# Kernel optimization log

Hardware: AMD Instinct MI355X
Metric: run time of the kernel (lower is better)

The kernel has to match this reference:

```python
import jax, jax.numpy as jnp
import numpy as np

BS, V, J = 256, 10475, 55
NSHAPE, NEXP = 300, 50

# SMPLX kinematic tree (fixed model constant)
PARENTS = np.array([
    -1, 0, 0, 0, 1, 2, 3, 4, 5, 6, 7, 8, 9, 9, 9, 12, 13, 14, 16, 17, 18, 19,
    15, 15, 15,
    20, 25, 26, 20, 28, 29, 20, 31, 32, 20, 34, 35, 20, 37, 38,
    21, 40, 41, 21, 43, 44, 21, 46, 47, 21, 49, 50, 21, 52, 53], dtype=np.int64)


def batch_rodrigues(rvec):
    # rvec: [N,3] axis-angle -> [N,3,3] rotation matrices
    angle = jnp.linalg.norm(rvec + 1e-8, axis=-1, keepdims=True)  # [N,1]
    axis = rvec / angle
    x, y, z = axis[..., 0], axis[..., 1], axis[..., 2]
    zr = jnp.zeros_like(x)
    K = jnp.stack([zr, -z, y, z, zr, -x, -y, x, zr], axis=-1).reshape(-1, 3, 3)
    s = jnp.sin(angle)[..., None]
    c = jnp.cos(angle)[..., None]
    I = jnp.eye(3, dtype=rvec.dtype)
    return I + s * K + (1.0 - c) * (K @ K)


def setup_inputs():
    key = jax.random.key(0)
    ks = jax.random.split(key, 9)
    pose = 0.2 * jax.random.normal(ks[0], (BS, 53, 3), jnp.float32)
    shape = jax.random.normal(ks[1], (BS, 10), jnp.float32)
    expression = jax.random.normal(ks[2], (BS, NEXP), jnp.float32)
    global_orient = 0.2 * jax.random.normal(ks[3], (1, 3), jnp.float32)
    v_template = jax.random.normal(ks[4], (V, 3), jnp.float32)
    shapedirs = 0.01 * jax.random.normal(ks[5], (V, 3, NSHAPE + NEXP), jnp.float32)
    posedirs = 0.01 * jax.random.normal(ks[6], (486, V * 3), jnp.float32)
    J_regressor = jax.random.uniform(ks[7], (J, V), jnp.float32)
    J_regressor = J_regressor / jnp.sum(J_regressor, axis=1, keepdims=True)
    lbs_weights = jax.random.uniform(ks[8], (V, J), jnp.float32)
    lbs_weights = lbs_weights / jnp.sum(lbs_weights, axis=1, keepdims=True)
    return {"pose": pose, "shape": shape, "expression": expression,
            "global_orient": global_orient, "v_template": v_template,
            "shapedirs": shapedirs, "posedirs": posedirs,
            "J_regressor": J_regressor, "lbs_weights": lbs_weights}


def lbs(betas, rot_mats, v_template, shapedirs, posedirs, J_regressor, lbs_weights):
    bs = betas.shape[0]
    dt = betas.dtype
    # shape blendshapes
    v_shaped = v_template[None] + jnp.einsum('bl,vcl->bvc', betas, shapedirs)
    # rest-pose joints
    joints = jnp.einsum('jv,bvc->bjc', J_regressor, v_shaped)  # [b,J,3]
    # pose blendshapes
    I3 = jnp.eye(3, dtype=dt)
    pose_feature = (rot_mats[:, 1:] - I3).reshape(bs, -1)  # [b,(J-1)*9]
    v_posed = v_shaped + jnp.einsum('bp,pn->bn', pose_feature, posedirs).reshape(bs, V, 3)
    # forward kinematics along the tree
    rel_joints = jnp.concatenate(
        [joints[:, :1], joints[:, 1:] - joints[:, PARENTS[1:]]], axis=1)
    top = jnp.concatenate([rot_mats, rel_joints[..., None]], axis=-1)  # [b,J,3,4]
    bot = jnp.broadcast_to(jnp.array([0, 0, 0, 1], dtype=dt), (bs, J, 1, 4))
    T_local = jnp.concatenate([top, bot], axis=-2)  # [b,J,4,4]
    A_list = [T_local[:, 0]]
    for j in range(1, J):  # fixed 55-joint chain
        A_list.append(A_list[int(PARENTS[j])] @ T_local[:, j])
    A = jnp.stack(A_list, axis=1)  # [b,J,4,4]
    posed_joints = A[..., :3, 3]
    # subtract rest-pose contribution
    corr = jnp.einsum('bjmn,bjn->bjm', A[..., :3, :3], joints)
    A_rel = A.at[..., :3, 3].add(-corr)
    # vertex skinning
    T = jnp.einsum('vj,bjmn->bvmn', lbs_weights, A_rel)  # [b,V,4,4]
    verts = jnp.einsum('bvmn,bvn->bvm', T[..., :3, :3], v_posed) + T[..., :3, 3]
    return verts, posed_joints


def reference(pose, shape, expression, global_orient, v_template, shapedirs,
              posedirs, J_regressor, lbs_weights):
    bs = pose.shape[0]
    dt = pose.dtype
    go = jnp.broadcast_to(global_orient[:, None, :], (bs, 1, 3))
    eyes = jnp.zeros((bs, 2, 3), dtype=dt)  # leye/reye fixed at zero
    # order: global, body(21), jaw, leye, reye, lhand(15), rhand(15) -> 55
    full_pose = jnp.concatenate(
        [go, pose[:, 1:22], pose[:, 52:53], eyes, pose[:, 22:37], pose[:, 37:52]],
        axis=1)
    betas = jnp.concatenate(
        [shape, jnp.zeros((bs, NSHAPE - shape.shape[1]), dtype=dt), expression],
        axis=1)  # [b,350]
    rot_mats = batch_rodrigues(full_pose.reshape(-1, 3)).reshape(bs, J, 3, 3)
    verts, joints = lbs(betas, rot_mats, v_template, shapedirs, posedirs,
                        J_regressor, lbs_weights)
    return verts, joints
```

## Files before the change

### kernel.cpp

```cpp
#include <hip/hip_runtime.h>
#include <math.h>

#define BS 256
#define V 10475
#define NJ 55
#define R3 31425
#define NP 486
#define LB 60
#define KP 576
#define VK 10496
#define JOFF 8044800

typedef __attribute__((ext_vector_type(8))) short short8;
typedef __attribute__((ext_vector_type(4))) float float4_;

__device__ const int PARENTS_d[NJ] = {
  -1, 0, 0, 0, 1, 2, 3, 4, 5, 6, 7, 8, 9, 9, 9, 12, 13, 14, 16, 17, 18, 19,
  15, 15, 15, 20, 25, 26, 20, 28, 29, 20, 31, 32, 20, 34, 35, 20, 37, 38,
  21, 40, 41, 21, 43, 44, 21, 46, 47, 21, 49, 50, 21, 52, 53
};

__device__ __forceinline__ unsigned short f2b(float f) {
  unsigned int u = __float_as_uint(f);
  unsigned int r = (u + 0x7FFFu + ((u >> 16) & 1u)) >> 16;
  return (unsigned short)r;
}

__global__ __launch_bounds__(256) void k_pose(
    const float* __restrict__ pose, const float* __restrict__ shp,
    const float* __restrict__ expr, const float* __restrict__ go,
    float* __restrict__ rot_ws, unsigned short* __restrict__ Ftr,
    float* __restrict__ betas_T) {
  int b = threadIdx.x;
  int j = blockIdx.x;
  if (j == NJ) {
    #pragma unroll
    for (int l = 0; l < 10; ++l) {
      float v = shp[b * 10 + l];
      betas_T[l * BS + b] = v;
      Ftr[(size_t)b * KP + NP + l] = f2b(v);
    }
    #pragma unroll
    for (int l = 0; l < 50; ++l) {
      float v = expr[b * 50 + l];
      betas_T[(10 + l) * BS + b] = v;
      Ftr[(size_t)b * KP + NP + 10 + l] = f2b(v);
    }
    #pragma unroll
    for (int l = NP + LB; l < KP; ++l) Ftr[(size_t)b * KP + l] = 0;
    return;
  }
  float rx, ry, rz;
  if (j == 0) { rx = go[0]; ry = go[1]; rz = go[2]; }
  else if (j == 23 || j == 24) { rx = 0.f; ry = 0.f; rz = 0.f; }
  else {
    int src = (j <= 21) ? j : (j == 22 ? 52 : j - 3);
    const float* p = pose + ((size_t)b * 53 + src) * 3;
    rx = p[0]; ry = p[1]; rz = p[2];
  }
  float sx = rx + 1e-8f, sy = ry + 1e-8f, sz = rz + 1e-8f;
  float ang = sqrtf(sx * sx + sy * sy + sz * sz);
  float inv = 1.f / ang;
  float x = rx * inv, y = ry * inv, z = rz * inv;
  float s = sinf(ang), c = cosf(ang), C = 1.f - c;
  float R[9];
  R[0] = 1.f - C * (y * y + z * z);
  R[1] = -s * z + C * x * y;
  R[2] =  s * y + C * x * z;
  R[3] =  s * z + C * x * y;
  R[4] = 1.f - C * (x * x + z * z);
  R[5] = -s * x + C * y * z;
  R[6] = -s * y + C * x * z;
  R[7] =  s * x + C * y * z;
  R[8] = 1.f - C * (x * x + y * y);
  float* rw = rot_ws + ((size_t)b * NJ + j) * 9;
  #pragma unroll
  for (int e = 0; e < 9; ++e) rw[e] = R[e];
  if (j >= 1) {
    int pb = (j - 1) * 9;
    #pragma unroll
    for (int e = 0; e < 9; ++e)
      Ftr[(size_t)b * KP + pb + e] =
          f2b(R[e] - ((e == 0 || e == 4 || e == 8) ? 1.f : 0.f));
  }
}

__global__ __launch_bounds__(256) void k_jregb(
    const float* __restrict__ Jreg, unsigned short* __restrict__ Jregb) {
  size_t idx = (size_t)blockIdx.x * 256 + threadIdx.x;
  int j = (int)(idx / VK);
  int v = (int)(idx - (size_t)j * VK);
  float val = (j < NJ && v < V) ? Jreg[(size_t)j * V + v] : 0.f;
  Jregb[idx] = f2b(val);
}

__global__ __launch_bounds__(256) void k_trX(
    const float* __restrict__ sd, const float* __restrict__ vt,
    unsigned short* __restrict__ XbT) {
  __shared__ float tile[192][65];
  int t = threadIdx.x;
  int v0 = blockIdx.x * 64;
  #pragma unroll 1
  for (int c = 0; c < 3; ++c) {
    for (int idx = t; idx < 3840; idx += 256) {
      int v_l = idx / 60, col = idx - v_l * 60;
      int v = v0 + v_l;
      int cidx = (col < 10) ? col : 290 + col;
      float val = (v < V) ? sd[((size_t)v * 3 + c) * 350 + cidx] : 0.f;
      tile[c * 64 + col][v_l] = val;
    }
  }
  for (int idx = t; idx < 768; idx += 256) {
    int v_l = idx & 63, rr = idx >> 6;
    int c = rr >> 2, l = 60 + (rr & 3);
    int v = v0 + v_l;
    float val = (l == 60 && v < V) ? vt[(size_t)v * 3 + c] : 0.f;
    tile[c * 64 + l][v_l] = val;
  }
  __syncthreads();
  for (int idx = t; idx < 192 * 64; idx += 256) {
    int cl = idx >> 6, v_l = idx & 63;
    XbT[(size_t)cl * VK + v0 + v_l] = f2b(tile[cl][v_l]);
  }
}

__global__ __launch_bounds__(256) void k_jsm(
    const unsigned short* __restrict__ Jregb,
    const unsigned short* __restrict__ XbT, float* __restrict__ JS) {
  int lane = threadIdx.x & 63;
  int wv = threadIdx.x >> 6;
  int l15 = lane & 15, q = lane >> 4;
  int k0 = blockIdx.x * 128;
  const unsigned short* ap = Jregb + (size_t)(wv * 16 + l15) * VK + k0 + q * 8;
  float4_ acc[12];
  #pragma unroll
  for (int nt = 0; nt < 12; ++nt) acc[nt] = (float4_)0.f;
  #pragma unroll
  for (int ks = 0; ks < 4; ++ks) {
    short8 a = *(const short8*)(ap + ks * 32);
    #pragma unroll
    for (int nt = 0; nt < 12; ++nt) {
      const unsigned short* bp =
          XbT + (size_t)(nt * 16 + l15) * VK + k0 + ks * 32 + q * 8;
      short8 b = *(const short8*)bp;
      acc[nt] = __builtin_amdgcn_mfma_f32_16x16x32_bf16(a, b, acc[nt], 0, 0, 0);
    }
  }
  #pragma unroll
  for (int nt = 0; nt < 12; ++nt) {
    int cl = nt * 16 + l15;
    int c = cl >> 6, l = cl & 63;
    if (l < 61) {
      #pragma unroll
      for (int reg = 0; reg < 4; ++reg) {
        int jj = wv * 16 + q * 4 + reg;
        if (jj < NJ)
          atomicAdd(&JS[((size_t)jj * 3 + c) * 61 + l], acc[nt][reg]);
      }
    }
  }
}

__global__ __launch_bounds__(256) void k_trD(
    const float* __restrict__ pd, const float* __restrict__ sd,
    unsigned short* __restrict__ Dtr) {
  __shared__ float tile[64 * 68];
  int t = threadIdx.x;
  int rt = blockIdx.x, kt = blockIdx.y;
  int r0 = rt * 64;
  int c = (t & 15) * 4;
  #pragma unroll
  for (int s = 0; s < 4; ++s) {
    int k_l = (t >> 4) + 16 * s;
    int kg = kt * 64 + k_l;
    float v0 = 0.f, v1 = 0.f, v2 = 0.f, v3 = 0.f;
    int r = r0 + c;
    if (kg < NP) {
      if (r + 3 < R3) {
        const float* p = pd + (size_t)kg * R3 + r;
        v0 = p[0]; v1 = p[1]; v2 = p[2]; v3 = p[3];
      } else {
        const float* p = pd + (size_t)kg * R3;
        if (r < R3)     v0 = p[r];
        if (r + 1 < R3) v1 = p[r + 1];
        if (r + 2 < R3) v2 = p[r + 2];
        if (r + 3 < R3) v3 = p[r + 3];
      }
    } else if (kg < NP + LB) {
      int ll = kg - NP;
      int cidx = (ll < 10) ? ll : (290 + ll);
      if (r < R3)     v0 = sd[(size_t)(r) * 350 + cidx];
      if (r + 1 < R3) v1 = sd[(size_t)(r + 1) * 350 + cidx];
      if (r + 2 < R3) v2 = sd[(size_t)(r + 2) * 350 + cidx];
      if (r + 3 < R3) v3 = sd[(size_t)(r + 3) * 350 + cidx];
    }
    float* tp = tile + k_l * 68 + c;
    tp[0] = v0; tp[1] = v1; tp[2] = v2; tp[3] = v3;
  }
  __syncthreads();
  int r_l = t >> 2, a = t & 3;
  unsigned short h[16];
  #pragma unroll
  for (int i = 0; i < 16; ++i) h[i] = f2b(tile[(a * 16 + i) * 68 + r_l]);
  unsigned short* dp = Dtr + (size_t)(r0 + r_l) * KP + kt * 64 + a * 16;
  #pragma unroll
  for (int i = 0; i < 16; ++i) dp[i] = h[i];
}

__global__ __launch_bounds__(256) void k_wb(
    const float* __restrict__ lbs, unsigned short* __restrict__ Wb) {
  int v0 = blockIdx.x * 16;
  for (int idx = threadIdx.x; idx < 1024; idx += 256) {
    int v_l = idx >> 6, k = idx & 63;
    int v = v0 + v_l;
    float val = (k < NJ && v < V) ? lbs[(size_t)v * NJ + k] : 0.f;
    Wb[(size_t)v * 64 + k] = f2b(val);
  }
}

__global__ __launch_bounds__(64) void k_chain(
    const float* __restrict__ JS, const float* __restrict__ betas_T,
    const float* __restrict__ rot_ws, unsigned short* __restrict__ arelb,
    float* __restrict__ out) {
  int b = blockIdx.x;
  int lane = threadIdx.x;
  __shared__ float joints_l[165];
  __shared__ float Tl[880];
  __shared__ float A[880];
  for (int idx = lane; idx < 165; idx += 64) {
    float sacc = JS[idx * 61 + 60];
    #pragma unroll
    for (int l = 0; l < LB; ++l) sacc += JS[idx * 61 + l] * betas_T[l * BS + b];
    joints_l[idx] = sacc;
  }
  __syncthreads();
  for (int idx = lane; idx < 880; idx += 64) {
    int j = idx >> 4, e = idx & 15, r = e >> 2, cc = e & 3;
    float val;
    if (r < 3) {
      if (cc < 3) val = rot_ws[((size_t)b * NJ + j) * 9 + r * 3 + cc];
      else {
        int par = PARENTS_d[j];
        val = joints_l[j * 3 + r] - (par >= 0 ? joints_l[par * 3 + r] : 0.f);
      }
    } else val = (cc == 3) ? 1.f : 0.f;
    Tl[idx] = val;
  }
  __syncthreads();
  if (lane < 16) A[lane] = Tl[lane];
  __syncthreads();
  for (int j = 1; j < NJ; ++j) {
    int par = PARENTS_d[j];
    if (lane < 16) {
      int r = lane >> 2, cc = lane & 3;
      float sacc = 0.f;
      #pragma unroll
      for (int k = 0; k < 4; ++k)
        sacc += A[par * 16 + r * 4 + k] * Tl[j * 16 + k * 4 + cc];
      A[j * 16 + lane] = sacc;
    }
    __syncthreads();
  }
  for (int idx = lane; idx < 165; idx += 64) {
    int j = idx / 3, r = idx % 3;
    out[JOFF + (size_t)b * 165 + idx] = A[j * 16 + r * 4 + 3];
  }
  for (int idx = lane; idx < 1024; idx += 64) {
    int n = idx >> 6, k = idx & 63;
    float val = 0.f;
    if (n < 12 && k < NJ) {
      int m = n >> 2, cc = n & 3;
      if (cc < 3) val = A[k * 16 + m * 4 + cc];
      else {
        val = A[k * 16 + m * 4 + 3]
            - (A[k * 16 + m * 4 + 0] * joints_l[k * 3 + 0] +
               A[k * 16 + m * 4 + 1] * joints_l[k * 3 + 1] +
               A[k * 16 + m * 4 + 2] * joints_l[k * 3 + 2]);
      }
    }
    arelb[(size_t)b * 1024 + idx] = f2b(val);
  }
}

__global__ __launch_bounds__(256) void k_gemm(
    const float* __restrict__ vt, const unsigned short* __restrict__ Ftr,
    const unsigned short* __restrict__ Dtr, float* __restrict__ out) {
  int lane = threadIdx.x & 63;
  int wv = threadIdx.x >> 6;
  int l15 = lane & 15, q = lane >> 4;
  int r0 = blockIdx.x * 64;
  int m0 = wv * 64;
  float4_ acc[4][4];
  #pragma unroll
  for (int mt = 0; mt < 4; ++mt)
    #pragma unroll
    for (int nt = 0; nt < 4; ++nt) acc[mt][nt] = (float4_)0.f;

  const unsigned short* aBase[4];
  const unsigned short* bBase[4];
  #pragma unroll
  for (int mt = 0; mt < 4; ++mt)
    aBase[mt] = Ftr + (size_t)(m0 + mt * 16 + l15) * KP + q * 8;
  #pragma unroll
  for (int nt = 0; nt < 4; ++nt)
    bBase[nt] = Dtr + (size_t)(r0 + nt * 16 + l15) * KP + q * 8;

  short8 af[4], bf[4], an[4], bn[4];
  #pragma unroll
  for (int mt = 0; mt < 4; ++mt) af[mt] = *(const short8*)(aBase[mt]);
  #pragma unroll
  for (int nt = 0; nt < 4; ++nt) bf[nt] = *(const short8*)(bBase[nt]);

  #pragma unroll 1
  for (int kk = 0; kk < 18; ++kk) {
    if (kk < 17) {
      int off = (kk + 1) * 32;
      #pragma unroll
      for (int mt = 0; mt < 4; ++mt) an[mt] = *(const short8*)(aBase[mt] + off);
      #pragma unroll
      for (int nt = 0; nt < 4; ++nt) bn[nt] = *(const short8*)(bBase[nt] + off);
    }
    #pragma unroll
    for (int mt = 0; mt < 4; ++mt)
      #pragma unroll
      for (int nt = 0; nt < 4; ++nt)
        acc[mt][nt] = __builtin_amdgcn_mfma_f32_16x16x32_bf16(
            af[mt], bf[nt], acc[mt][nt], 0, 0, 0);
    #pragma unroll
    for (int mt = 0; mt < 4; ++mt) af[mt] = an[mt];
    #pragma unroll
    for (int nt = 0; nt < 4; ++nt) bf[nt] = bn[nt];
  }

  #pragma unroll
  for (int nt = 0; nt < 4; ++nt) {
    int r = r0 + nt * 16 + l15;
    if (r < R3) {
      float vtv = vt[r];
      #pragma unroll
      for (int mt = 0; mt < 4; ++mt) {
        int bb = m0 + mt * 16 + q * 4;
        #pragma unroll
        for (int reg = 0; reg < 4; ++reg)
          out[(size_t)(bb + reg) * R3 + r] = acc[mt][nt][reg] + vtv;
      }
    }
  }
}

__global__ __launch_bounds__(256) void k_skin(
    const unsigned short* __restrict__ Wb, const unsigned short* __restrict__ arelb,
    float* __restrict__ out) {
  __shared__ float Tls[4 * 320];
  int lane = threadIdx.x & 63;
  int wv = threadIdx.x >> 6;
  int l15 = lane & 15, q = lane >> 4;
  int v0 = blockIdx.x * 16;
  int bbase = blockIdx.y * 64 + wv * 16;
  float* tb = Tls + wv * 320;

  const unsigned short* wp = Wb + (size_t)(v0 + l15) * 64 + q * 8;
  short8 a0 = *(const short8*)(wp);
  short8 a1 = *(const short8*)(wp + 32);

  int v = v0 + l15;
  int m = q;
  #pragma unroll 1
  for (int bi = 0; bi < 16; ++bi) {
    int b = bbase + bi;
    const unsigned short* bp = arelb + (size_t)b * 1024 + l15 * 64 + q * 8;
    short8 b0 = *(const short8*)(bp);
    short8 b1 = *(const short8*)(bp + 32);
    float4_ acc = (float4_)0.f;
    acc = __builtin_amdgcn_mfma_f32_16x16x32_bf16(a0, b0, acc, 0, 0, 0);
    acc = __builtin_amdgcn_mfma_f32_16x16x32_bf16(a1, b1, acc, 0, 0, 0);
    #pragma unroll
    for (int reg = 0; reg < 4; ++reg) tb[(q * 4 + reg) * 20 + l15] = acc[reg];
    __builtin_amdgcn_s_waitcnt(0);
    float4_ T4 = *(float4_*)(&tb[l15 * 20 + m * 4]);
    if (m < 3 && v < V) {
      float* vp = out + (size_t)b * R3 + v * 3;
      float x = vp[0], y = vp[1], z = vp[2];
      float val = T4[0] * x + T4[1] * y + T4[2] * z + T4[3];
      vp[m] = val;
    }
  }
}

extern "C" void kernel_launch(void* const* d_in, const int* in_sizes, int n_in,
                              void* d_out, int out_size, void* d_ws, size_t ws_size,
                              hipStream_t stream) {
  const float* pose = (const float*)d_in[0];
  const float* shp  = (const float*)d_in[1];
  const float* expr = (const float*)d_in[2];
  const float* go   = (const float*)d_in[3];
  const float* vt   = (const float*)d_in[4];
  const float* sd   = (const float*)d_in[5];
  const float* pd   = (const float*)d_in[6];
  const float* jr   = (const float*)d_in[7];
  const float* lbs  = (const float*)d_in[8];
  float* out = (float*)d_out;
  float* ws  = (float*)d_ws;

  float* betas_T        = ws;
  float* rot_ws         = ws + 15360;
  float* JS             = ws + 142080;
  unsigned short* Ftr   = (unsigned short*)(ws + 152160);
  unsigned short* arelb = (unsigned short*)(ws + 225888);
  unsigned short* Wb    = (unsigned short*)(ws + 356960);
  unsigned short* Jregb = (unsigned short*)(ws + 692320);
  unsigned short* XbT   = (unsigned short*)(ws + 1028192);
  unsigned short* Dtr   = (unsigned short*)(ws + 2035808);

  hipMemsetAsync(JS, 0, 10080 * sizeof(float), stream);
  k_pose<<<NJ + 1, 256, 0, stream>>>(pose, shp, expr, go, rot_ws, Ftr, betas_T);
  k_jregb<<<(64 * VK) / 256, 256, 0, stream>>>(jr, Jregb);
  k_trX<<<VK / 64, 256, 0, stream>>>(sd, vt, XbT);
  k_jsm<<<VK / 128, 256, 0, stream>>>(Jregb, XbT, JS);
  k_trD<<<dim3(492, 9), 256, 0, stream>>>(pd, sd, Dtr);
  k_wb<<<655, 256, 0, stream>>>(lbs, Wb);
  k_chain<<<BS, 64, 0, stream>>>(JS, betas_T, rot_ws, arelb, out);
  k_gemm<<<492, 256, 0, stream>>>(vt, Ftr, Dtr, out);
  k_skin<<<dim3(655, 4), 256, 0, stream>>>(Wb, arelb, out);
}
```

Baseline: 337.6 us.

## Fuse posedirs transpose into GEMM via LDS double-buffer and restructure skinning

Drops the separate k_trD kernel that wrote a bf16 transposed copy of posedirs and shapedirs. The GEMM now streams fp32 posedirs/shapedirs tiles straight into double-buffered shared memory and converts them to bf16 as it builds the MFMA operands, which removes one full write and re-read of the intermediate. The skinning kernel is also reorganised: four waves cover different vertices, the next bone-transform fragment is prefetched, and the MFMA result is used directly instead of going through shared memory. The cost is a __syncthreads per K chunk and strided uncoalesced shapedirs reads inside the GEMM, and k_wb is enlarged so Wb covers padded vertices.

```diff
diff --git a/kernel.cpp b/kernel.cpp
--- a/kernel.cpp
+++ b/kernel.cpp
@@ -10,6 +10,7 @@
 #define KP 576
 #define VK 10496
 #define JOFF 8044800
+#define DSP 66
 
 typedef __attribute__((ext_vector_type(8))) short short8;
 typedef __attribute__((ext_vector_type(4))) float float4_;
@@ -161,52 +162,6 @@
   }
 }
 
-__global__ __launch_bounds__(256) void k_trD(
-    const float* __restrict__ pd, const float* __restrict__ sd,
-    unsigned short* __restrict__ Dtr) {
-  __shared__ float tile[64 * 68];
-  int t = threadIdx.x;
-  int rt = blockIdx.x, kt = blockIdx.y;
-  int r0 = rt * 64;
-  int c = (t & 15) * 4;
-  #pragma unroll
-  for (int s = 0; s < 4; ++s) {
-    int k_l = (t >> 4) + 16 * s;
-    int kg = kt * 64 + k_l;
-    float v0 = 0.f, v1 = 0.f, v2 = 0.f, v3 = 0.f;
-    int r = r0 + c;
-    if (kg < NP) {
-      if (r + 3 < R3) {
-        const float* p = pd + (size_t)kg * R3 + r;
-        v0 = p[0]; v1 = p[1]; v2 = p[2]; v3 = p[3];
-      } else {
-        const float* p = pd + (size_t)kg * R3;
-        if (r < R3)     v0 = p[r];
-        if (r + 1 < R3) v1 = p[r + 1];
-        if (r + 2 < R3) v2 = p[r + 2];
-        if (r + 3 < R3) v3 = p[r + 3];
-      }
-    } else if (kg < NP + LB) {
-      int ll = kg - NP;
-      int cidx = (ll < 10) ? ll : (290 + ll);
-      if (r < R3)     v0 = sd[(size_t)(r) * 350 + cidx];
-      if (r + 1 < R3) v1 = sd[(size_t)(r + 1) * 350 + cidx];
-      if (r + 2 < R3) v2 = sd[(size_t)(r + 2) * 350 + cidx];
-      if (r + 3 < R3) v3 = sd[(size_t)(r + 3) * 350 + cidx];
-    }
-    float* tp = tile + k_l * 68 + c;
-    tp[0] = v0; tp[1] = v1; tp[2] = v2; tp[3] = v3;
-  }
-  __syncthreads();
-  int r_l = t >> 2, a = t & 3;
-  unsigned short h[16];
-  #pragma unroll
-  for (int i = 0; i < 16; ++i) h[i] = f2b(tile[(a * 16 + i) * 68 + r_l]);
-  unsigned short* dp = Dtr + (size_t)(r0 + r_l) * KP + kt * 64 + a * 16;
-  #pragma unroll
-  for (int i = 0; i < 16; ++i) dp[i] = h[i];
-}
-
 __global__ __launch_bounds__(256) void k_wb(
     const float* __restrict__ lbs, unsigned short* __restrict__ Wb) {
   int v0 = blockIdx.x * 16;
@@ -214,7 +169,7 @@
     int v_l = idx >> 6, k = idx & 63;
     int v = v0 + v_l;
     float val = (k < NJ && v < V) ? lbs[(size_t)v * NJ + k] : 0.f;
-    Wb[(size_t)v * 64 + k] = f2b(val);
+    if (v < VK) Wb[(size_t)v * 64 + k] = f2b(val);
   }
 }
 
@@ -283,13 +238,19 @@
 }
 
 __global__ __launch_bounds__(256) void k_gemm(
-    const float* __restrict__ vt, const unsigned short* __restrict__ Ftr,
-    const unsigned short* __restrict__ Dtr, float* __restrict__ out) {
-  int lane = threadIdx.x & 63;
-  int wv = threadIdx.x >> 6;
+    const float* __restrict__ vt, const float* __restrict__ sd,
+    const float* __restrict__ pd, const unsigned short* __restrict__ Ftr,
+    float* __restrict__ out) {
+  __shared__ float dsb[2][32 * DSP];
+  int t = threadIdx.x;
+  int lane = t & 63, wv = t >> 6;
   int l15 = lane & 15, q = lane >> 4;
   int r0 = blockIdx.x * 64;
   int m0 = wv * 64;
+  int k_l = t >> 3;
+  int c8 = (t & 7) * 8;
+  bool full = (r0 + 64 <= R3);
+
   float4_ acc[4][4];
   #pragma unroll
   for (int mt = 0; mt < 4; ++mt)
@@ -297,39 +258,86 @@
     for (int nt = 0; nt < 4; ++nt) acc[mt][nt] = (float4_)0.f;
 
   const unsigned short* aBase[4];
-  const unsigned short* bBase[4];
   #pragma unroll
   for (int mt = 0; mt < 4; ++mt)
     aBase[mt] = Ftr + (size_t)(m0 + mt * 16 + l15) * KP + q * 8;
-  #pragma unroll
-  for (int nt = 0; nt < 4; ++nt)
-    bBase[nt] = Dtr + (size_t)(r0 + nt * 16 + l15) * KP + q * 8;
-
-  short8 af[4], bf[4], an[4], bn[4];
-  #pragma unroll
-  for (int mt = 0; mt < 4; ++mt) af[mt] = *(const short8*)(aBase[mt]);
-  #pragma unroll
-  for (int nt = 0; nt < 4; ++nt) bf[nt] = *(const short8*)(bBase[nt]);
+
+  {
+    int kg = k_l;
+    float* dp = &dsb[0][k_l * DSP + c8];
+    if (full) {
+      const float* p = pd + (size_t)kg * R3 + r0 + c8;
+      #pragma unroll
+      for (int i = 0; i < 8; ++i) dp[i] = p[i];
+    } else {
+      #pragma unroll
+      for (int i = 0; i < 8; ++i) {
+        int r = r0 + c8 + i;
+        dp[i] = (r < R3) ? pd[(size_t)kg * R3 + r] : 0.f;
+      }
+    }
+  }
+  __syncthreads();
 
   #pragma unroll 1
-  for (int kk = 0; kk < 18; ++kk) {
-    if (kk < 17) {
-      int off = (kk + 1) * 32;
-      #pragma unroll
-      for (int mt = 0; mt < 4; ++mt) an[mt] = *(const short8*)(aBase[mt] + off);
-      #pragma unroll
-      for (int nt = 0; nt < 4; ++nt) bn[nt] = *(const short8*)(bBase[nt] + off);
-    }
+  for (int c = 0; c < 18; ++c) {
+    int cur = c & 1;
+    float sv[8];
+    if (c < 17) {
+      int kg = (c + 1) * 32 + k_l;
+      if (kg < NP) {
+        if (full) {
+          const float* p = pd + (size_t)kg * R3 + r0 + c8;
+          #pragma unroll
+          for (int i = 0; i < 8; ++i) sv[i] = p[i];
+        } else {
+          #pragma unroll
+          for (int i = 0; i < 8; ++i) {
+            int r = r0 + c8 + i;
+            sv[i] = (r < R3) ? pd[(size_t)kg * R3 + r] : 0.f;
+          }
+        }
+      } else if (kg < NP + LB) {
+        int ll = kg - NP;
+        int cidx = (ll < 10) ? ll : (290 + ll);
+        #pragma unroll
+        for (int i = 0; i < 8; ++i) {
+          int r = r0 + c8 + i;
+          sv[i] = (r < R3) ? sd[(size_t)r * 350 + cidx] : 0.f;
+        }
+      } else {
+        #pragma unroll
+        for (int i = 0; i < 8; ++i) sv[i] = 0.f;
+      }
+    }
+    short8 bf[4];
+    #pragma unroll
+    for (int nt = 0; nt < 4; ++nt) {
+      unsigned short h[8];
+      #pragma unroll
+      for (int i = 0; i < 8; ++i)
+        h[i] = f2b(dsb[cur][(q * 8 + i) * DSP + nt * 16 + l15]);
+      short8 v;
+      #pragma unroll
+      for (int i = 0; i < 8; ++i) v[i] = (short)h[i];
+      bf[nt] = v;
+    }
+    short8 af[4];
+    #pragma unroll
+    for (int mt = 0; mt < 4; ++mt)
+      af[mt] = *(const short8*)(aBase[mt] + c * 32);
     #pragma unroll
     for (int mt = 0; mt < 4; ++mt)
       #pragma unroll
       for (int nt = 0; nt < 4; ++nt)
         acc[mt][nt] = __builtin_amdgcn_mfma_f32_16x16x32_bf16(
             af[mt], bf[nt], acc[mt][nt], 0, 0, 0);
-    #pragma unroll
-    for (int mt = 0; mt < 4; ++mt) af[mt] = an[mt];
-    #pragma unroll
-    for (int nt = 0; nt < 4; ++nt) bf[nt] = bn[nt];
+    if (c < 17) {
+      float* dp = &dsb[cur ^ 1][k_l * DSP + c8];
+      #pragma unroll
+      for (int i = 0; i < 8; ++i) dp[i] = sv[i];
+    }
+    __syncthreads();
   }
 
   #pragma unroll
@@ -351,39 +359,39 @@
 __global__ __launch_bounds__(256) void k_skin(
     const unsigned short* __restrict__ Wb, const unsigned short* __restrict__ arelb,
     float* __restrict__ out) {
-  __shared__ float Tls[4 * 320];
   int lane = threadIdx.x & 63;
   int wv = threadIdx.x >> 6;
   int l15 = lane & 15, q = lane >> 4;
-  int v0 = blockIdx.x * 16;
-  int bbase = blockIdx.y * 64 + wv * 16;
-  float* tb = Tls + wv * 320;
-
-  const unsigned short* wp = Wb + (size_t)(v0 + l15) * 64 + q * 8;
-  short8 a0 = *(const short8*)(wp);
-  short8 a1 = *(const short8*)(wp + 32);
-
-  int v = v0 + l15;
-  int m = q;
+  int v = blockIdx.x * 64 + wv * 16 + l15;
+  bool vok = (v < V);
+  int b0 = blockIdx.y * 16;
+
+  const unsigned short* wp = Wb + (size_t)v * 64 + q * 8;
+  short8 w0 = *(const short8*)(wp);
+  short8 w1 = *(const short8*)(wp + 32);
+
+  const unsigned short* ap = arelb + (size_t)b0 * 1024 + l15 * 64 + q * 8;
+  short8 a0 = *(const short8*)ap;
+  short8 a1 = *(const short8*)(ap + 32);
+
   #pragma unroll 1
   for (int bi = 0; bi < 16; ++bi) {
-    int b = bbase + bi;
-    const unsigned short* bp = arelb + (size_t)b * 1024 + l15 * 64 + q * 8;
-    short8 b0 = *(const short8*)(bp);
-    short8 b1 = *(const short8*)(bp + 32);
+    int b = b0 + bi;
+    float* vp = out + (size_t)b * R3 + v * 3;
+    float x = 0.f, y = 0.f, z = 0.f;
+    if (vok && q < 3) { x = vp[0]; y = vp[1]; z = vp[2]; }
+    short8 na0 = a0, na1 = a1;
+    if (bi < 15) {
+      const unsigned short* np = arelb + (size_t)(b + 1) * 1024 + l15 * 64 + q * 8;
+      na0 = *(const short8*)np;
+      na1 = *(const short8*)(np + 32);
+    }
     float4_ acc = (float4_)0.f;
-    acc = __builtin_amdgcn_mfma_f32_16x16x32_bf16(a0, b0, acc, 0, 0, 0);
-    acc = __builtin_amdgcn_mfma_f32_16x16x32_bf16(a1, b1, acc, 0, 0, 0);
-    #pragma unroll
-    for (int reg = 0; reg < 4; ++reg) tb[(q * 4 + reg) * 20 + l15] = acc[reg];
-    __builtin_amdgcn_s_waitcnt(0);
-    float4_ T4 = *(float4_*)(&tb[l15 * 20 + m * 4]);
-    if (m < 3 && v < V) {
-      float* vp = out + (size_t)b * R3 + v * 3;
-      float x = vp[0], y = vp[1], z = vp[2];
-      float val = T4[0] * x + T4[1] * y + T4[2] * z + T4[3];
-      vp[m] = val;
-    }
+    acc = __builtin_amdgcn_mfma_f32_16x16x32_bf16(a0, w0, acc, 0, 0, 0);
+    acc = __builtin_amdgcn_mfma_f32_16x16x32_bf16(a1, w1, acc, 0, 0, 0);
+    if (vok && q < 3)
+      vp[q] = acc[0] * x + acc[1] * y + acc[2] * z + acc[3];
+    a0 = na0; a1 = na1;
   }
 }
 
@@ -408,18 +416,16 @@
   unsigned short* Ftr   = (unsigned short*)(ws + 152160);
   unsigned short* arelb = (unsigned short*)(ws + 225888);
   unsigned short* Wb    = (unsigned short*)(ws + 356960);
-  unsigned short* Jregb = (unsigned short*)(ws + 692320);
-  unsigned short* XbT   = (unsigned short*)(ws + 1028192);
-  unsigned short* Dtr   = (unsigned short*)(ws + 2035808);
+  unsigned short* Jregb = (unsigned short*)(ws + 692832);
+  unsigned short* XbT   = (unsigned short*)(ws + 1028704);
 
   hipMemsetAsync(JS, 0, 10080 * sizeof(float), stream);
   k_pose<<<NJ + 1, 256, 0, stream>>>(pose, shp, expr, go, rot_ws, Ftr, betas_T);
   k_jregb<<<(64 * VK) / 256, 256, 0, stream>>>(jr, Jregb);
   k_trX<<<VK / 64, 256, 0, stream>>>(sd, vt, XbT);
   k_jsm<<<VK / 128, 256, 0, stream>>>(Jregb, XbT, JS);
-  k_trD<<<dim3(492, 9), 256, 0, stream>>>(pd, sd, Dtr);
-  k_wb<<<655, 256, 0, stream>>>(lbs, Wb);
+  k_wb<<<VK / 16, 256, 0, stream>>>(lbs, Wb);
   k_chain<<<BS, 64, 0, stream>>>(JS, betas_T, rot_ws, arelb, out);
-  k_gemm<<<492, 256, 0, stream>>>(vt, Ftr, Dtr, out);
-  k_skin<<<dim3(655, 4), 256, 0, stream>>>(Wb, arelb, out);
-}
+  k_gemm<<<492, 256, 0, stream>>>(vt, sd, pd, Ftr, out);
+  k_skin<<<dim3(164, 16), 256, 0, stream>>>(Wb, arelb, out);
+}
```

Result: faster. 311.4 us (-7.8%).

## Fuse preprocessing kernels, replace JS atomics with split-K reduction, rework skinning

Applied to the files above, without the earlier changes.

Merges the pose, Jregb, XbT, Wb and Dtr preprocessing kernels into one launch that dispatches on block index. The joint-regressor GEMM now writes per-block partial sums to a workspace, and a separate reduction kernel replaces the memset and the float atomics. The skinning kernel swaps the shared-memory round trip for wave shuffles, uses coalesced per-component output indexing and prefetches the next batch's inputs. The trade-offs are extra workspace traffic for the partials, one more launch for the reduction, and a larger fused grid with mixed block work.

```diff
diff --git a/kernel.cpp b/kernel.cpp
--- a/kernel.cpp
+++ b/kernel.cpp
@@ -10,6 +10,18 @@
 #define KP 576
 #define VK 10496
 #define JOFF 8044800
+#define NKSPLIT 164
+
+#define NB_POSE 56
+#define NB_JREGB 2624
+#define NB_TRX 164
+#define NB_WB 656
+#define NB_TRD 4428
+#define B0_JREGB (NB_POSE)
+#define B0_TRX (B0_JREGB + NB_JREGB)
+#define B0_WB (B0_TRX + NB_TRX)
+#define B0_TRD (B0_WB + NB_WB)
+#define NB_PRE (B0_TRD + NB_TRD)
 
 typedef __attribute__((ext_vector_type(8))) short short8;
 typedef __attribute__((ext_vector_type(4))) float float4_;
@@ -26,117 +38,167 @@
   return (unsigned short)r;
 }
 
-__global__ __launch_bounds__(256) void k_pose(
+__global__ __launch_bounds__(256) void k_pre(
     const float* __restrict__ pose, const float* __restrict__ shp,
     const float* __restrict__ expr, const float* __restrict__ go,
+    const float* __restrict__ Jreg, const float* __restrict__ lbs,
+    const float* __restrict__ sd, const float* __restrict__ vt,
+    const float* __restrict__ pd,
     float* __restrict__ rot_ws, unsigned short* __restrict__ Ftr,
-    float* __restrict__ betas_T) {
-  int b = threadIdx.x;
-  int j = blockIdx.x;
-  if (j == NJ) {
-    #pragma unroll
-    for (int l = 0; l < 10; ++l) {
-      float v = shp[b * 10 + l];
-      betas_T[l * BS + b] = v;
-      Ftr[(size_t)b * KP + NP + l] = f2b(v);
-    }
-    #pragma unroll
-    for (int l = 0; l < 50; ++l) {
-      float v = expr[b * 50 + l];
-      betas_T[(10 + l) * BS + b] = v;
-      Ftr[(size_t)b * KP + NP + 10 + l] = f2b(v);
-    }
-    #pragma unroll
-    for (int l = NP + LB; l < KP; ++l) Ftr[(size_t)b * KP + l] = 0;
-    return;
-  }
-  float rx, ry, rz;
-  if (j == 0) { rx = go[0]; ry = go[1]; rz = go[2]; }
-  else if (j == 23 || j == 24) { rx = 0.f; ry = 0.f; rz = 0.f; }
-  else {
-    int src = (j <= 21) ? j : (j == 22 ? 52 : j - 3);
-    const float* p = pose + ((size_t)b * 53 + src) * 3;
-    rx = p[0]; ry = p[1]; rz = p[2];
-  }
-  float sx = rx + 1e-8f, sy = ry + 1e-8f, sz = rz + 1e-8f;
-  float ang = sqrtf(sx * sx + sy * sy + sz * sz);
-  float inv = 1.f / ang;
-  float x = rx * inv, y = ry * inv, z = rz * inv;
-  float s = sinf(ang), c = cosf(ang), C = 1.f - c;
-  float R[9];
-  R[0] = 1.f - C * (y * y + z * z);
-  R[1] = -s * z + C * x * y;
-  R[2] =  s * y + C * x * z;
-  R[3] =  s * z + C * x * y;
-  R[4] = 1.f - C * (x * x + z * z);
-  R[5] = -s * x + C * y * z;
-  R[6] = -s * y + C * x * z;
-  R[7] =  s * x + C * y * z;
-  R[8] = 1.f - C * (x * x + y * y);
-  float* rw = rot_ws + ((size_t)b * NJ + j) * 9;
-  #pragma unroll
-  for (int e = 0; e < 9; ++e) rw[e] = R[e];
-  if (j >= 1) {
-    int pb = (j - 1) * 9;
-    #pragma unroll
-    for (int e = 0; e < 9; ++e)
-      Ftr[(size_t)b * KP + pb + e] =
-          f2b(R[e] - ((e == 0 || e == 4 || e == 8) ? 1.f : 0.f));
-  }
-}
-
-__global__ __launch_bounds__(256) void k_jregb(
-    const float* __restrict__ Jreg, unsigned short* __restrict__ Jregb) {
-  size_t idx = (size_t)blockIdx.x * 256 + threadIdx.x;
-  int j = (int)(idx / VK);
-  int v = (int)(idx - (size_t)j * VK);
-  float val = (j < NJ && v < V) ? Jreg[(size_t)j * V + v] : 0.f;
-  Jregb[idx] = f2b(val);
-}
-
-__global__ __launch_bounds__(256) void k_trX(
-    const float* __restrict__ sd, const float* __restrict__ vt,
-    unsigned short* __restrict__ XbT) {
-  __shared__ float tile[192][65];
+    float* __restrict__ betas_T, unsigned short* __restrict__ Jregb,
+    unsigned short* __restrict__ Wb, unsigned short* __restrict__ XbT,
+    unsigned short* __restrict__ Dtr) {
+  __shared__ float smem[64 * 68];
+  int blk = blockIdx.x;
   int t = threadIdx.x;
-  int v0 = blockIdx.x * 64;
-  #pragma unroll 1
-  for (int c = 0; c < 3; ++c) {
-    for (int idx = t; idx < 3840; idx += 256) {
-      int v_l = idx / 60, col = idx - v_l * 60;
+
+  if (blk < NB_POSE) {
+    int b = t;
+    int j = blk;
+    if (j == NJ) {
+      #pragma unroll
+      for (int l = 0; l < 10; ++l) {
+        float v = shp[b * 10 + l];
+        betas_T[l * BS + b] = v;
+        Ftr[(size_t)b * KP + NP + l] = f2b(v);
+      }
+      #pragma unroll
+      for (int l = 0; l < 50; ++l) {
+        float v = expr[b * 50 + l];
+        betas_T[(10 + l) * BS + b] = v;
+        Ftr[(size_t)b * KP + NP + 10 + l] = f2b(v);
+      }
+      #pragma unroll
+      for (int l = NP + LB; l < KP; ++l) Ftr[(size_t)b * KP + l] = 0;
+      return;
+    }
+    float rx, ry, rz;
+    if (j == 0) { rx = go[0]; ry = go[1]; rz = go[2]; }
+    else if (j == 23 || j == 24) { rx = 0.f; ry = 0.f; rz = 0.f; }
+    else {
+      int src = (j <= 21) ? j : (j == 22 ? 52 : j - 3);
+      const float* p = pose + ((size_t)b * 53 + src) * 3;
+      rx = p[0]; ry = p[1]; rz = p[2];
+    }
+    float sx = rx + 1e-8f, sy = ry + 1e-8f, sz = rz + 1e-8f;
+    float ang = sqrtf(sx * sx + sy * sy + sz * sz);
+    float inv = 1.f / ang;
+    float x = rx * inv, y = ry * inv, z = rz * inv;
+    float s = sinf(ang), c = cosf(ang), C = 1.f - c;
+    float R[9];
+    R[0] = 1.f - C * (y * y + z * z);
+    R[1] = -s * z + C * x * y;
+    R[2] =  s * y + C * x * z;
+    R[3] =  s * z + C * x * y;
+    R[4] = 1.f - C * (x * x + z * z);
+    R[5] = -s * x + C * y * z;
+    R[6] = -s * y + C * x * z;
+    R[7] =  s * x + C * y * z;
+    R[8] = 1.f - C * (x * x + y * y);
+    float* rw = rot_ws + ((size_t)b * NJ + j) * 9;
+    #pragma unroll
+    for (int e = 0; e < 9; ++e) rw[e] = R[e];
+    if (j >= 1) {
+      int pb = (j - 1) * 9;
+      #pragma unroll
+      for (int e = 0; e < 9; ++e)
+        Ftr[(size_t)b * KP + pb + e] =
+            f2b(R[e] - ((e == 0 || e == 4 || e == 8) ? 1.f : 0.f));
+    }
+  } else if (blk < B0_TRX) {
+    size_t idx = (size_t)(blk - B0_JREGB) * 256 + t;
+    int j = (int)(idx / VK);
+    int v = (int)(idx - (size_t)j * VK);
+    float val = (j < NJ && v < V) ? Jreg[(size_t)j * V + v] : 0.f;
+    Jregb[idx] = f2b(val);
+  } else if (blk < B0_WB) {
+    int v0 = (blk - B0_TRX) * 64;
+    #pragma unroll 1
+    for (int c = 0; c < 3; ++c) {
+      for (int idx = t; idx < 3840; idx += 256) {
+        int v_l = idx / 60, col = idx - v_l * 60;
+        int v = v0 + v_l;
+        int cidx = (col < 10) ? col : 290 + col;
+        smem[col * 65 + v_l] = (v < V) ? sd[((size_t)v * 3 + c) * 350 + cidx] : 0.f;
+      }
+      {
+        int v_l = t & 63, rr = t >> 6;
+        int v = v0 + v_l;
+        smem[(60 + rr) * 65 + v_l] =
+            (rr == 0 && v < V) ? vt[(size_t)v * 3 + c] : 0.f;
+      }
+      __syncthreads();
+      for (int idx = t; idx < 4096; idx += 256) {
+        int cl = idx >> 6, v_l = idx & 63;
+        XbT[(size_t)(c * 64 + cl) * VK + v0 + v_l] = f2b(smem[cl * 65 + v_l]);
+      }
+      __syncthreads();
+    }
+  } else if (blk < B0_TRD) {
+    int v0 = (blk - B0_WB) * 16;
+    for (int idx = t; idx < 1024; idx += 256) {
+      int v_l = idx >> 6, k = idx & 63;
       int v = v0 + v_l;
-      int cidx = (col < 10) ? col : 290 + col;
-      float val = (v < V) ? sd[((size_t)v * 3 + c) * 350 + cidx] : 0.f;
-      tile[c * 64 + col][v_l] = val;
-    }
-  }
-  for (int idx = t; idx < 768; idx += 256) {
-    int v_l = idx & 63, rr = idx >> 6;
-    int c = rr >> 2, l = 60 + (rr & 3);
-    int v = v0 + v_l;
-    float val = (l == 60 && v < V) ? vt[(size_t)v * 3 + c] : 0.f;
-    tile[c * 64 + l][v_l] = val;
-  }
-  __syncthreads();
-  for (int idx = t; idx < 192 * 64; idx += 256) {
-    int cl = idx >> 6, v_l = idx & 63;
-    XbT[(size_t)cl * VK + v0 + v_l] = f2b(tile[cl][v_l]);
+      float val = (k < NJ && v < V) ? lbs[(size_t)v * NJ + k] : 0.f;
+      if (v < VK) Wb[(size_t)v * 64 + k] = f2b(val);
+    }
+  } else {
+    int b2 = blk - B0_TRD;
+    int rt = b2 % 492, kt = b2 / 492;
+    int r0 = rt * 64;
+    int c = (t & 15) * 4;
+    #pragma unroll
+    for (int s = 0; s < 4; ++s) {
+      int k_l = (t >> 4) + 16 * s;
+      int kg = kt * 64 + k_l;
+      float v0 = 0.f, v1 = 0.f, v2 = 0.f, v3 = 0.f;
+      int r = r0 + c;
+      if (kg < NP) {
+        if (r + 3 < R3) {
+          const float* p = pd + (size_t)kg * R3 + r;
+          v0 = p[0]; v1 = p[1]; v2 = p[2]; v3 = p[3];
+        } else {
+          const float* p = pd + (size_t)kg * R3;
+          if (r < R3)     v0 = p[r];
+          if (r + 1 < R3) v1 = p[r + 1];
+          if (r + 2 < R3) v2 = p[r + 2];
+          if (r + 3 < R3) v3 = p[r + 3];
+        }
+      } else if (kg < NP + LB) {
+        int ll = kg - NP;
+        int cidx = (ll < 10) ? ll : (290 + ll);
+        if (r < R3)     v0 = sd[(size_t)(r) * 350 + cidx];
+        if (r + 1 < R3) v1 = sd[(size_t)(r + 1) * 350 + cidx];
+        if (r + 2 < R3) v2 = sd[(size_t)(r + 2) * 350 + cidx];
+        if (r + 3 < R3) v3 = sd[(size_t)(r + 3) * 350 + cidx];
+      }
+      float* tp = smem + k_l * 68 + c;
+      tp[0] = v0; tp[1] = v1; tp[2] = v2; tp[3] = v3;
+    }
+    __syncthreads();
+    int r_l = t >> 2, a = t & 3;
+    unsigned short h[16];
+    #pragma unroll
+    for (int i = 0; i < 16; ++i) h[i] = f2b(smem[(a * 16 + i) * 68 + r_l]);
+    unsigned short* dp = Dtr + (size_t)(r0 + r_l) * KP + kt * 64 + a * 16;
+    #pragma unroll
+    for (int i = 0; i < 16; ++i) dp[i] = h[i];
   }
 }
 
 __global__ __launch_bounds__(256) void k_jsm(
     const unsigned short* __restrict__ Jregb,
-    const unsigned short* __restrict__ XbT, float* __restrict__ JS) {
+    const unsigned short* __restrict__ XbT, float* __restrict__ Ppart) {
   int lane = threadIdx.x & 63;
   int wv = threadIdx.x >> 6;
   int l15 = lane & 15, q = lane >> 4;
-  int k0 = blockIdx.x * 128;
+  int k0 = blockIdx.x * 64;
   const unsigned short* ap = Jregb + (size_t)(wv * 16 + l15) * VK + k0 + q * 8;
   float4_ acc[12];
   #pragma unroll
   for (int nt = 0; nt < 12; ++nt) acc[nt] = (float4_)0.f;
   #pragma unroll
-  for (int ks = 0; ks < 4; ++ks) {
+  for (int ks = 0; ks < 2; ++ks) {
     short8 a = *(const short8*)(ap + ks * 32);
     #pragma unroll
     for (int nt = 0; nt < 12; ++nt) {
@@ -146,6 +208,7 @@
       acc[nt] = __builtin_amdgcn_mfma_f32_16x16x32_bf16(a, b, acc[nt], 0, 0, 0);
     }
   }
+  float* pp = Ppart + (size_t)blockIdx.x * 10080;
   #pragma unroll
   for (int nt = 0; nt < 12; ++nt) {
     int cl = nt * 16 + l15;
@@ -154,68 +217,20 @@
       #pragma unroll
       for (int reg = 0; reg < 4; ++reg) {
         int jj = wv * 16 + q * 4 + reg;
-        if (jj < NJ)
-          atomicAdd(&JS[((size_t)jj * 3 + c) * 61 + l], acc[nt][reg]);
-      }
-    }
-  }
-}
-
-__global__ __launch_bounds__(256) void k_trD(
-    const float* __restrict__ pd, const float* __restrict__ sd,
-    unsigned short* __restrict__ Dtr) {
-  __shared__ float tile[64 * 68];
-  int t = threadIdx.x;
-  int rt = blockIdx.x, kt = blockIdx.y;
-  int r0 = rt * 64;
-  int c = (t & 15) * 4;
-  #pragma unroll
-  for (int s = 0; s < 4; ++s) {
-    int k_l = (t >> 4) + 16 * s;
-    int kg = kt * 64 + k_l;
-    float v0 = 0.f, v1 = 0.f, v2 = 0.f, v3 = 0.f;
-    int r = r0 + c;
-    if (kg < NP) {
-      if (r + 3 < R3) {
-        const float* p = pd + (size_t)kg * R3 + r;
-        v0 = p[0]; v1 = p[1]; v2 = p[2]; v3 = p[3];
-      } else {
-        const float* p = pd + (size_t)kg * R3;
-        if (r < R3)     v0 = p[r];
-        if (r + 1 < R3) v1 = p[r + 1];
-        if (r + 2 < R3) v2 = p[r + 2];
-        if (r + 3 < R3) v3 = p[r + 3];
-      }
-    } else if (kg < NP + LB) {
-      int ll = kg - NP;
-      int cidx = (ll < 10) ? ll : (290 + ll);
-      if (r < R3)     v0 = sd[(size_t)(r) * 350 + cidx];
-      if (r + 1 < R3) v1 = sd[(size_t)(r + 1) * 350 + cidx];
-      if (r + 2 < R3) v2 = sd[(size_t)(r + 2) * 350 + cidx];
-      if (r + 3 < R3) v3 = sd[(size_t)(r + 3) * 350 + cidx];
-    }
-    float* tp = tile + k_l * 68 + c;
-    tp[0] = v0; tp[1] = v1; tp[2] = v2; tp[3] = v3;
-  }
-  __syncthreads();
-  int r_l = t >> 2, a = t & 3;
-  unsigned short h[16];
-  #pragma unroll
-  for (int i = 0; i < 16; ++i) h[i] = f2b(tile[(a * 16 + i) * 68 + r_l]);
-  unsigned short* dp = Dtr + (size_t)(r0 + r_l) * KP + kt * 64 + a * 16;
-  #pragma unroll
-  for (int i = 0; i < 16; ++i) dp[i] = h[i];
-}
-
-__global__ __launch_bounds__(256) void k_wb(
-    const float* __restrict__ lbs, unsigned short* __restrict__ Wb) {
-  int v0 = blockIdx.x * 16;
-  for (int idx = threadIdx.x; idx < 1024; idx += 256) {
-    int v_l = idx >> 6, k = idx & 63;
-    int v = v0 + v_l;
-    float val = (k < NJ && v < V) ? lbs[(size_t)v * NJ + k] : 0.f;
-    Wb[(size_t)v * 64 + k] = f2b(val);
-  }
+        if (jj < NJ) pp[((size_t)jj * 3 + c) * 61 + l] = acc[nt][reg];
+      }
+    }
+  }
+}
+
+__global__ __launch_bounds__(256) void k_jsred(
+    const float* __restrict__ Ppart, float* __restrict__ JS) {
+  int idx = blockIdx.x * 256 + threadIdx.x;
+  if (idx >= 10065) return;
+  float s = 0.f;
+  #pragma unroll 4
+  for (int p = 0; p < NKSPLIT; ++p) s += Ppart[(size_t)p * 10080 + idx];
+  JS[idx] = s;
 }
 
 __global__ __launch_bounds__(64) void k_chain(
@@ -351,39 +366,52 @@
 __global__ __launch_bounds__(256) void k_skin(
     const unsigned short* __restrict__ Wb, const unsigned short* __restrict__ arelb,
     float* __restrict__ out) {
-  __shared__ float Tls[4 * 320];
   int lane = threadIdx.x & 63;
   int wv = threadIdx.x >> 6;
   int l15 = lane & 15, q = lane >> 4;
-  int v0 = blockIdx.x * 16;
-  int bbase = blockIdx.y * 64 + wv * 16;
-  float* tb = Tls + wv * 320;
-
-  const unsigned short* wp = Wb + (size_t)(v0 + l15) * 64 + q * 8;
-  short8 a0 = *(const short8*)(wp);
-  short8 a1 = *(const short8*)(wp + 32);
-
-  int v = v0 + l15;
-  int m = q;
+  int v0w = blockIdx.x * 64 + wv * 16;
+  int b0 = blockIdx.y * 16;
+
+  const unsigned short* wp = Wb + (size_t)(v0w + l15) * 64 + q * 8;
+  short8 w0 = *(const short8*)(wp);
+  short8 w1 = *(const short8*)(wp + 32);
+
+  int vi = lane / 3;
+  int ci = lane - vi * 3;
+  int srcT = ci * 16 + (vi & 15);
+  int srcX = vi * 3 <= 63 ? vi * 3 : 63;
+  int r = v0w * 3 + lane;
+  bool rok = (lane < 48) && (r < R3);
+
+  float vload = 0.f;
+  if (rok) vload = out[(size_t)b0 * R3 + r];
+  const unsigned short* ap = arelb + (size_t)b0 * 1024 + l15 * 64 + q * 8;
+  short8 a0 = *(const short8*)ap;
+  short8 a1 = *(const short8*)(ap + 32);
+
   #pragma unroll 1
   for (int bi = 0; bi < 16; ++bi) {
-    int b = bbase + bi;
-    const unsigned short* bp = arelb + (size_t)b * 1024 + l15 * 64 + q * 8;
-    short8 b0 = *(const short8*)(bp);
-    short8 b1 = *(const short8*)(bp + 32);
+    int b = b0 + bi;
+    float nvload = 0.f;
+    short8 na0 = a0, na1 = a1;
+    if (bi < 15) {
+      if (rok) nvload = out[(size_t)(b + 1) * R3 + r];
+      const unsigned short* np = arelb + (size_t)(b + 1) * 1024 + l15 * 64 + q * 8;
+      na0 = *(const short8*)np;
+      na1 = *(const short8*)(np + 32);
+    }
     float4_ acc = (float4_)0.f;
-    acc = __builtin_amdgcn_mfma_f32_16x16x32_bf16(a0, b0, acc, 0, 0, 0);
-    acc = __builtin_amdgcn_mfma_f32_16x16x32_bf16(a1, b1, acc, 0, 0, 0);
-    #pragma unroll
-    for (int reg = 0; reg < 4; ++reg) tb[(q * 4 + reg) * 20 + l15] = acc[reg];
-    __builtin_amdgcn_s_waitcnt(0);
-    float4_ T4 = *(float4_*)(&tb[l15 * 20 + m * 4]);
-    if (m < 3 && v < V) {
-      float* vp = out + (size_t)b * R3 + v * 3;
-      float x = vp[0], y = vp[1], z = vp[2];
-      float val = T4[0] * x + T4[1] * y + T4[2] * z + T4[3];
-      vp[m] = val;
-    }
+    acc = __builtin_amdgcn_mfma_f32_16x16x32_bf16(a0, w0, acc, 0, 0, 0);
+    acc = __builtin_amdgcn_mfma_f32_16x16x32_bf16(a1, w1, acc, 0, 0, 0);
+    float T0 = __shfl(acc[0], srcT, 64);
+    float T1 = __shfl(acc[1], srcT, 64);
+    float T2 = __shfl(acc[2], srcT, 64);
+    float T3 = __shfl(acc[3], srcT, 64);
+    float x = __shfl(vload, srcX, 64);
+    float y = __shfl(vload, srcX + 1 <= 63 ? srcX + 1 : 63, 64);
+    float z = __shfl(vload, srcX + 2 <= 63 ? srcX + 2 : 63, 64);
+    if (rok) out[(size_t)b * R3 + r] = T0 * x + T1 * y + T2 * z + T3;
+    vload = nvload; a0 = na0; a1 = na1;
   }
 }
 
@@ -408,18 +436,16 @@
   unsigned short* Ftr   = (unsigned short*)(ws + 152160);
   unsigned short* arelb = (unsigned short*)(ws + 225888);
   unsigned short* Wb    = (unsigned short*)(ws + 356960);
-  unsigned short* Jregb = (unsigned short*)(ws + 692320);
-  unsigned short* XbT   = (unsigned short*)(ws + 1028192);
-  unsigned short* Dtr   = (unsigned short*)(ws + 2035808);
-
-  hipMemsetAsync(JS, 0, 10080 * sizeof(float), stream);
-  k_pose<<<NJ + 1, 256, 0, stream>>>(pose, shp, expr, go, rot_ws, Ftr, betas_T);
-  k_jregb<<<(64 * VK) / 256, 256, 0, stream>>>(jr, Jregb);
-  k_trX<<<VK / 64, 256, 0, stream>>>(sd, vt, XbT);
-  k_jsm<<<VK / 128, 256, 0, stream>>>(Jregb, XbT, JS);
-  k_trD<<<dim3(492, 9), 256, 0, stream>>>(pd, sd, Dtr);
-  k_wb<<<655, 256, 0, stream>>>(lbs, Wb);
+  unsigned short* Jregb = (unsigned short*)(ws + 692832);
+  unsigned short* XbT   = (unsigned short*)(ws + 1028704);
+  unsigned short* Dtr   = (unsigned short*)(ws + 2036320);
+  float* Ppart          = ws + 11104864;
+
+  k_pre<<<NB_PRE, 256, 0, stream>>>(pose, shp, expr, go, jr, lbs, sd, vt, pd,
+                                    rot_ws, Ftr, betas_T, Jregb, Wb, XbT, Dtr);
+  k_jsm<<<NKSPLIT, 256, 0, stream>>>(Jregb, XbT, Ppart);
+  k_jsred<<<40, 256, 0, stream>>>(Ppart, JS);
   k_chain<<<BS, 64, 0, stream>>>(JS, betas_T, rot_ws, arelb, out);
   k_gemm<<<492, 256, 0, stream>>>(vt, Ftr, Dtr, out);
-  k_skin<<<dim3(655, 4), 256, 0, stream>>>(Wb, arelb, out);
-}
+  k_skin<<<dim3(164, 16), 256, 0, stream>>>(Wb, arelb, out);
+}
```

Measured after the change: 296.4 us. -12.2%, faster.
